# Kernel optimization log

Hardware: AMD Instinct MI355X
Metric: run time of the kernel (lower is better)

Reference implementation:

```python
import jax, jax.numpy as jnp
import numpy as np


def _lstm_layer(x, w_ih, w_hh, b, h0, c0):
    # x: [S, B, H]; w_ih, w_hh: [4H, H]; b: [4H] (b_ih + b_hh combined)
    H = h0.shape[-1]

    def step(carry, xt):
        h, c = carry
        gates = xt @ w_ih.T + h @ w_hh.T + b  # [B, 4H]
        i = jax.nn.sigmoid(gates[:, 0 * H:1 * H])
        f = jax.nn.sigmoid(gates[:, 1 * H:2 * H])
        g = jnp.tanh(gates[:, 2 * H:3 * H])
        o = jax.nn.sigmoid(gates[:, 3 * H:4 * H])
        c = f * c + i * g
        h = o * jnp.tanh(c)
        return (h, c), h

    (_, _), hs = jax.lax.scan(step, (h0, c0), x)
    return hs  # [S, B, H]


def setup_inputs() -> dict:
    key = jax.random.key(0)
    ks = jax.random.split(key, 5)
    S, B, H, L, C = 256, 64, 1024, 2, 10
    return {
        "x_data": jax.random.normal(ks[0], (S, B, H), dtype=jnp.float32),
        "weight": jax.random.normal(ks[1], (L, 2, 4 * H, H), dtype=jnp.float32) * 0.05,
        "bias": jax.random.normal(ks[2], (L, 2, 4 * H), dtype=jnp.float32) * 0.05,
        "fc_w": jax.random.normal(ks[3], (C, H), dtype=jnp.float32) * 0.05,
        "fc_b": jax.random.normal(ks[4], (C,), dtype=jnp.float32) * 0.05,
        "hiddenSize": H,
        "miniBatch": B,
        "seqLength": S,
        "numLayers": L,
    }


def reference(x_data, weight, bias, fc_w, fc_b, hiddenSize, miniBatch, seqLength, numLayers):
    B, H = miniBatch, hiddenSize
    h0 = jnp.zeros((B, H), dtype=x_data.dtype)
    c0 = jnp.zeros((B, H), dtype=x_data.dtype)
    x = x_data
    for layer in range(numLayers):
        w_ih = weight[layer, 0]  # [4H, H]
        w_hh = weight[layer, 1]  # [4H, H]
        b = bias[layer, 0] + bias[layer, 1]  # [4H]
        x = _lstm_layer(x, w_ih, w_hh, b, h0, c0)
    out = x[-1]  # last timestep of top layer: [B, H]
    return out @ fc_w.T + fc_b  # [B, num_classes]
```

## Files before the change

### kernel.cpp

```cpp
#include <hip/hip_runtime.h>
#include <cstdint>
#include <cstddef>

#define S_LEN 256
#define BATCH 64
#define HID   1024
#define GATES 4096
#define NBLK  256
#define RING_D 4
#define FLAG_STRIDE 32

typedef _Float16 h16;
typedef _Float16 h16x8 __attribute__((ext_vector_type(8)));
typedef _Float16 h16x4 __attribute__((ext_vector_type(4)));
typedef float    f32x4 __attribute__((ext_vector_type(4)));

__global__ __launch_bounds__(256)
void xconv_kernel(const float* __restrict__ x, h16* __restrict__ x16)
{
  const int n4 = S_LEN * BATCH * HID / 4;
  const int stride = gridDim.x * 256;
  for (int i = blockIdx.x * 256 + threadIdx.x; i < n4; i += stride) {
    f32x4 v = ((const f32x4*)x)[i];
    h16x4 o;
    o[0] = (h16)v[0]; o[1] = (h16)v[1]; o[2] = (h16)v[2]; o[3] = (h16)v[3];
    ((h16x4*)x16)[i] = o;
  }
}

#define RLOAD(dst, ptr, OFFSTR)                                         \
  asm volatile("global_load_dwordx4 %0, %1, off offset:" OFFSTR " sc1"  \
               : "=&v"(dst) : "v"(ptr) : "memory")

__global__ __launch_bounds__(512, 1)
void lstm_persistent(const h16* __restrict__ x16,
                     const float* __restrict__ weight,
                     const float* __restrict__ bias,
                     h16* __restrict__ h0r,
                     h16* __restrict__ h1r,
                     unsigned* __restrict__ flags)
{
  __shared__ h16   wlds[65536];
  __shared__ float plds[8][16][32];

  const int wg    = blockIdx.x;
  const int layer = wg >> 7;
  const int j0    = (wg & 127) * 8;
  const int tid   = threadIdx.x;
  const int wave  = tid >> 6, lane = tid & 63;
  const int l15   = lane & 15, l16 = lane >> 4;
  const int BH    = BATCH * HID;

  {
    const float* wsrc = weight + (size_t)layer * 2 * GATES * HID;
    for (int c = tid; c < 8192; c += 512) {
      const int ln = c & 63, s = (c >> 6) & 3, n2 = (c >> 8) & 1,
                w = (c >> 9) & 7, part = c >> 12;
      const int lc  = n2 * 16 + (ln & 15);
      const int col = (lc >> 3) * HID + j0 + (lc & 7);
      const int k   = w * 128 + s * 32 + (ln >> 4) * 8;
      const float* p = wsrc + (part ? (size_t)GATES * HID : (size_t)0)
                            + (size_t)col * HID + k;
      h16x8 v;
#pragma unroll
      for (int e = 0; e < 8; ++e) v[e] = (h16)p[e];
      *(h16x8*)&wlds[(size_t)c * 8] = v;
    }
  }
  float bc[4];
  {
    const int j = tid & 7;
#pragma unroll
    for (int gg = 0; gg < 4; ++gg) {
      const int col = gg * HID + j0 + j;
      bc[gg] = bias[(size_t)layer * 2 * GATES + col] +
               bias[(size_t)layer * 2 * GATES + GATES + col];
    }
  }
  float creg[4] = {0.f, 0.f, 0.f, 0.f};
  __syncthreads();

  const int own_base = layer * 128;
  const int oth_base = (1 - layer) * 128;
  const h16* bbI = wlds + (size_t)wave * 4096 + lane * 8;
  const h16* bbH = bbI + 32768;
  const int kw = wave * 128 + l16 * 8;

  for (int t = 0; t < S_LEN; ++t) {
    const h16* As;
    if (layer == 0) {
      As = x16 + (size_t)t * BH;
    } else {
      if (tid >= 128 && tid < 256) {
        const unsigned tg = (unsigned)(t + 1);
        while (__hip_atomic_load(&flags[(oth_base + tid - 128) * FLAG_STRIDE],
                                 __ATOMIC_RELAXED,
                                 __HIP_MEMORY_SCOPE_AGENT) < tg) {}
      }
      __syncthreads();
      As = h0r + (size_t)(t % RING_D) * BH;
    }

    f32x4 accI[4][2];
#pragma unroll
    for (int i = 0; i < 4; ++i)
#pragma unroll
      for (int n2 = 0; n2 < 2; ++n2) accI[i][n2] = (f32x4)0.f;

#pragma unroll
    for (int sc = 0; sc < 2; ++sc) {
      h16x8 aS[2][4];
      if (layer == 0) {
#pragma unroll
        for (int ss = 0; ss < 2; ++ss)
#pragma unroll
          for (int i = 0; i < 4; ++i)
            aS[ss][i] = *(const h16x8*)(As + (size_t)(i * 16 + l15) * HID +
                                        kw + (sc * 2 + ss) * 32);
      } else {
#pragma unroll
        for (int i = 0; i < 4; ++i) {
          const h16* ap = As + (size_t)(i * 16 + l15) * HID + kw + sc * 64;
          RLOAD(aS[0][i], ap, "0");
          RLOAD(aS[1][i], ap, "64");
        }
        asm volatile("s_waitcnt vmcnt(0)" ::: "memory");
        __builtin_amdgcn_sched_barrier(0);
      }
#pragma unroll
      for (int ss = 0; ss < 2; ++ss) {
        const int s = sc * 2 + ss;
        const h16x8 b0 = *(const h16x8*)(bbI + s * 512);
        const h16x8 b1 = *(const h16x8*)(bbI + 2048 + s * 512);
#pragma unroll
        for (int i = 0; i < 4; ++i) {
          accI[i][0] = __builtin_amdgcn_mfma_f32_16x16x32_f16(aS[ss][i], b0, accI[i][0], 0, 0, 0);
          accI[i][1] = __builtin_amdgcn_mfma_f32_16x16x32_f16(aS[ss][i], b1, accI[i][1], 0, 0, 0);
        }
      }
    }

    if (tid < 128) {
      if (t) {
        const unsigned tg = (unsigned)t;
        while (__hip_atomic_load(&flags[(own_base + tid) * FLAG_STRIDE],
                                 __ATOMIC_RELAXED,
                                 __HIP_MEMORY_SCOPE_AGENT) < tg) {}
      }
    } else if (tid < 256 && layer == 0) {
      const int ct = t + 1 - RING_D;
      if (ct > 0) {
        const unsigned tg = (unsigned)ct;
        while (__hip_atomic_load(&flags[(oth_base + tid - 128) * FLAG_STRIDE],
                                 __ATOMIC_RELAXED,
                                 __HIP_MEMORY_SCOPE_AGENT) < tg) {}
      }
    }
    __syncthreads();

    const h16* Ah;
    h16* Hout;
    if (layer == 0) {
      Ah   = h0r + (size_t)((t + RING_D - 1) % RING_D) * BH;
      Hout = h0r + (size_t)(t % RING_D) * BH;
    } else {
      Ah   = h1r + (size_t)((t + 1) & 1) * BH;
      Hout = h1r + (size_t)(t & 1) * BH;
    }

    h16x8 aH[4][4];
#pragma unroll
    for (int i = 0; i < 4; ++i) {
      const h16* ap = Ah + (size_t)(i * 16 + l15) * HID + kw;
      RLOAD(aH[i][0], ap, "0");
      RLOAD(aH[i][1], ap, "64");
      RLOAD(aH[i][2], ap, "128");
      RLOAD(aH[i][3], ap, "192");
    }
    asm volatile("s_waitcnt vmcnt(0)" ::: "memory");
    __builtin_amdgcn_sched_barrier(0);

    f32x4 acc[4][2];
#pragma unroll
    for (int i = 0; i < 4; ++i)
#pragma unroll
      for (int n2 = 0; n2 < 2; ++n2) acc[i][n2] = accI[i][n2];

#pragma unroll
    for (int s = 0; s < 4; ++s) {
      const h16x8 b0 = *(const h16x8*)(bbH + s * 512);
      const h16x8 b1 = *(const h16x8*)(bbH + 2048 + s * 512);
#pragma unroll
      for (int i = 0; i < 4; ++i) {
        acc[i][0] = __builtin_amdgcn_mfma_f32_16x16x32_f16(aH[i][s], b0, acc[i][0], 0, 0, 0);
        acc[i][1] = __builtin_amdgcn_mfma_f32_16x16x32_f16(aH[i][s], b1, acc[i][1], 0, 0, 0);
      }
    }

#pragma unroll
    for (int i = 0; i < 4; ++i) {
#pragma unroll
      for (int n2 = 0; n2 < 2; ++n2)
#pragma unroll
        for (int q = 0; q < 4; ++q) {
          const int r = l16 * 4 + q;
          const int colS = (n2 * 16 + l15) ^ ((r & 7) << 2);
          plds[wave][r][colS] = acc[i][n2][q];
        }
      __syncthreads();
      if (tid < 128) {
        const int r = tid >> 3, j = tid & 7;
        float gv[4];
#pragma unroll
        for (int gg = 0; gg < 4; ++gg) {
          const int colS = (gg * 8 + j) ^ ((r & 7) << 2);
          float s = bc[gg];
#pragma unroll
          for (int w = 0; w < 8; ++w) s += plds[w][r][colS];
          gv[gg] = s;
        }
        const float ig = 1.f / (1.f + __expf(-gv[0]));
        const float fg = 1.f / (1.f + __expf(-gv[1]));
        const float gt = 1.f - 2.f / (__expf(2.f * gv[2]) + 1.f);
        const float og = 1.f / (1.f + __expf(-gv[3]));
        const float cn = fg * creg[i] + ig * gt;
        creg[i] = cn;
        const float th = 1.f - 2.f / (__expf(2.f * cn) + 1.f);
        union { h16 f; unsigned short u; } hb;
        hb.f = (h16)(og * th);
        __hip_atomic_store(
            (unsigned short*)&Hout[(size_t)(i * 16 + r) * HID + j0 + j],
            hb.u, __ATOMIC_RELAXED, __HIP_MEMORY_SCOPE_AGENT);
      }
      __syncthreads();
    }

    if (tid == 0)
      __hip_atomic_store(&flags[wg * FLAG_STRIDE], (unsigned)(t + 1),
                         __ATOMIC_RELAXED, __HIP_MEMORY_SCOPE_AGENT);
  }
}

__global__ __launch_bounds__(256)
void fc_kernel(const h16* __restrict__ h,
               const float* __restrict__ fw,
               const float* __restrict__ fb,
               float* __restrict__ out)
{
  const int gw = (blockIdx.x * blockDim.x + threadIdx.x) >> 6;
  const int lane = threadIdx.x & 63;
  if (gw >= BATCH * 10) return;
  const int m = gw / 10, cls = gw % 10;
  float s = 0.f;
  for (int k = lane; k < HID; k += 64)
    s += (float)h[(size_t)m * HID + k] * fw[(size_t)cls * HID + k];
#pragma unroll
  for (int off = 32; off; off >>= 1) s += __shfl_down(s, off);
  if (lane == 0) out[m * 10 + cls] = s + fb[cls];
}

extern "C" void kernel_launch(void* const* d_in, const int* in_sizes, int n_in,
                              void* d_out, int out_size, void* d_ws, size_t ws_size,
                              hipStream_t stream)
{
  const float* x      = (const float*)d_in[0];
  const float* weight = (const float*)d_in[1];
  const float* bias   = (const float*)d_in[2];
  const float* fc_w   = (const float*)d_in[3];
  const float* fc_b   = (const float*)d_in[4];
  float* out = (float*)d_out;

  auto align = [](size_t v) { return (v + 255) & ~(size_t)255; };
  const size_t flags_sz = (size_t)NBLK * FLAG_STRIDE * sizeof(unsigned);
  const size_t x16_sz   = (size_t)S_LEN * BATCH * HID * sizeof(h16);
  const size_t h0r_sz   = (size_t)RING_D * BATCH * HID * sizeof(h16);
  const size_t h1r_sz   = (size_t)2 * BATCH * HID * sizeof(h16);

  char* p = (char*)d_ws;
  unsigned* flags = (unsigned*)p; p += align(flags_sz);
  h16* x16 = (h16*)p; p += align(x16_sz);
  h16* h0r = (h16*)p; p += align(h0r_sz);
  h16* h1r = (h16*)p; p += align(h1r_sz);

  hipMemsetAsync(flags, 0, flags_sz, stream);
  hipMemsetAsync(h0r, 0, h0r_sz, stream);
  hipMemsetAsync(h1r, 0, h1r_sz, stream);

  xconv_kernel<<<dim3(2048), 256, 0, stream>>>(x, x16);

  lstm_persistent<<<dim3(NBLK), dim3(512), 0, stream>>>(
      x16, weight, bias, h0r, h1r, flags);

  fc_kernel<<<dim3((BATCH * 10 * 64) / 256), 256, 0, stream>>>(
      h1r + (size_t)BATCH * HID, fc_w, fc_b, out);
}
```

Baseline: 2.702 ms.

## Poll flags per wave with sleep and halve epilogue barrier rounds

Every wave now polls the dependency flags itself, checking 128 flags with two loads per lane and backing off with s_sleep. This removes the block-wide __syncthreads that used to follow a poll done by a subset of threads. The gate epilogue now stages two 16-row batch slices in LDS per round and uses 256 threads instead of 128, so it needs two barrier rounds instead of four. In exchange, all waves generate flag-polling memory traffic, and s_sleep can add wake-up latency after a flag flips.

```diff
diff --git a/kernel.cpp b/kernel.cpp
--- a/kernel.cpp
+++ b/kernel.cpp
@@ -32,6 +32,16 @@
   asm volatile("global_load_dwordx4 %0, %1, off offset:" OFFSTR " sc1"  \
                : "=&v"(dst) : "v"(ptr) : "memory")
 
+__device__ __forceinline__ void wave_poll(const unsigned* flags, int base,
+                                          unsigned tgt, int lane)
+{
+  const unsigned* f0 = &flags[(size_t)(base + lane) * FLAG_STRIDE];
+  const unsigned* f1 = &flags[(size_t)(base + 64 + lane) * FLAG_STRIDE];
+  while (__hip_atomic_load(f0, __ATOMIC_RELAXED, __HIP_MEMORY_SCOPE_AGENT) < tgt ||
+         __hip_atomic_load(f1, __ATOMIC_RELAXED, __HIP_MEMORY_SCOPE_AGENT) < tgt)
+    __builtin_amdgcn_s_sleep(1);
+}
+
 __global__ __launch_bounds__(512, 1)
 void lstm_persistent(const h16* __restrict__ x16,
                      const float* __restrict__ weight,
@@ -41,7 +51,7 @@
                      unsigned* __restrict__ flags)
 {
   __shared__ h16   wlds[65536];
-  __shared__ float plds[8][16][32];
+  __shared__ float plds[2][8][16][32];
 
   const int wg    = blockIdx.x;
   const int layer = wg >> 7;
@@ -77,7 +87,7 @@
                bias[(size_t)layer * 2 * GATES + GATES + col];
     }
   }
-  float creg[4] = {0.f, 0.f, 0.f, 0.f};
+  float creg2[2] = {0.f, 0.f};
   __syncthreads();
 
   const int own_base = layer * 128;
@@ -91,13 +101,7 @@
     if (layer == 0) {
       As = x16 + (size_t)t * BH;
     } else {
-      if (tid >= 128 && tid < 256) {
-        const unsigned tg = (unsigned)(t + 1);
-        while (__hip_atomic_load(&flags[(oth_base + tid - 128) * FLAG_STRIDE],
-                                 __ATOMIC_RELAXED,
-                                 __HIP_MEMORY_SCOPE_AGENT) < tg) {}
-      }
-      __syncthreads();
+      wave_poll(flags, oth_base, (unsigned)(t + 1), lane);
       As = h0r + (size_t)(t % RING_D) * BH;
     }
 
@@ -140,23 +144,11 @@
       }
     }
 
-    if (tid < 128) {
-      if (t) {
-        const unsigned tg = (unsigned)t;
-        while (__hip_atomic_load(&flags[(own_base + tid) * FLAG_STRIDE],
-                                 __ATOMIC_RELAXED,
-                                 __HIP_MEMORY_SCOPE_AGENT) < tg) {}
-      }
-    } else if (tid < 256 && layer == 0) {
+    if (t) wave_poll(flags, own_base, (unsigned)t, lane);
+    if (layer == 0) {
       const int ct = t + 1 - RING_D;
-      if (ct > 0) {
-        const unsigned tg = (unsigned)ct;
-        while (__hip_atomic_load(&flags[(oth_base + tid - 128) * FLAG_STRIDE],
-                                 __ATOMIC_RELAXED,
-                                 __HIP_MEMORY_SCOPE_AGENT) < tg) {}
-      }
-    }
-    __syncthreads();
+      if (ct > 0) wave_poll(flags, oth_base, (unsigned)ct, lane);
+    }
 
     const h16* Ah;
     h16* Hout;
@@ -198,38 +190,43 @@
     }
 
 #pragma unroll
-    for (int i = 0; i < 4; ++i) {
-#pragma unroll
-      for (int n2 = 0; n2 < 2; ++n2)
-#pragma unroll
-        for (int q = 0; q < 4; ++q) {
-          const int r = l16 * 4 + q;
-          const int colS = (n2 * 16 + l15) ^ ((r & 7) << 2);
-          plds[wave][r][colS] = acc[i][n2][q];
-        }
+    for (int p = 0; p < 2; ++p) {
+#pragma unroll
+      for (int ii = 0; ii < 2; ++ii) {
+        const int i = p * 2 + ii;
+#pragma unroll
+        for (int n2 = 0; n2 < 2; ++n2)
+#pragma unroll
+          for (int q = 0; q < 4; ++q) {
+            const int r = l16 * 4 + q;
+            const int colS = (n2 * 16 + l15) ^ ((r & 7) << 2);
+            plds[ii][wave][r][colS] = acc[i][n2][q];
+          }
+      }
       __syncthreads();
-      if (tid < 128) {
-        const int r = tid >> 3, j = tid & 7;
+      if (tid < 256) {
+        const int ii = tid >> 7, r = (tid >> 3) & 15, j = tid & 7;
         float gv[4];
 #pragma unroll
         for (int gg = 0; gg < 4; ++gg) {
           const int colS = (gg * 8 + j) ^ ((r & 7) << 2);
           float s = bc[gg];
 #pragma unroll
-          for (int w = 0; w < 8; ++w) s += plds[w][r][colS];
+        for (int w = 0; w < 8; ++w) s += plds[ii][w][r][colS];
           gv[gg] = s;
         }
         const float ig = 1.f / (1.f + __expf(-gv[0]));
         const float fg = 1.f / (1.f + __expf(-gv[1]));
         const float gt = 1.f - 2.f / (__expf(2.f * gv[2]) + 1.f);
         const float og = 1.f / (1.f + __expf(-gv[3]));
-        const float cn = fg * creg[i] + ig * gt;
-        creg[i] = cn;
+        const float cn = fg * creg2[p] + ig * gt;
+        creg2[p] = cn;
         const float th = 1.f - 2.f / (__expf(2.f * cn) + 1.f);
         union { h16 f; unsigned short u; } hb;
         hb.f = (h16)(og * th);
+        const int row = (p * 2 + ii) * 16 + r;
         __hip_atomic_store(
-            (unsigned short*)&Hout[(size_t)(i * 16 + r) * HID + j0 + j],
+            (unsigned short*)&Hout[(size_t)row * HID + j0 + j],
             hb.u, __ATOMIC_RELAXED, __HIP_MEMORY_SCOPE_AGENT);
       }
       __syncthreads();
```

New measurement: 2.637 ms. 2.4% less time.
